# Kernel tuning notes

Hardware: AMD Instinct MI355X
Metric: run time of the kernel (lower is better)

## Reference

```python
import jax, jax.numpy as jnp
import numpy as np

B, S, E, H, MAXLEN = 2, 2048, 1024, 16, 2048


def _level_indices(seq_len: int, base: int = 2) -> np.ndarray:
    """Vectorized version of get_level_index_weak over the full (target, source) grid.
    indices[t, s] = min(level, 2) for s < t, else 0. Runs in O(log S) passes."""
    tt = np.broadcast_to(np.arange(seq_len)[:, None], (seq_len, seq_len)).astype(np.int64).copy()
    ss = np.broadcast_to(np.arange(seq_len)[None, :], (seq_len, seq_len)).astype(np.int64).copy()
    res = np.zeros((seq_len, seq_len), np.int64)
    done = ~(ss < tt)  # only source < target positions get a level; rest stay 0
    while not done.all():
        l = np.floor(np.log2(np.maximum(tt, 1).astype(np.float64))).astype(np.int64)
        v = (np.int64(1) << l)
        hit = (~done) & (ss < v)
        res[hit] = l[hit] + 1
        done |= hit
        step = ~done
        tt[step] -= v[step]
        ss[step] -= v[step]
    return np.minimum(res, 2).astype(np.int32)


def setup_inputs() -> dict:
    key = jax.random.key(0)
    ks = jax.random.split(key, 10)
    sc = 0.02
    return {
        "x": jax.random.normal(ks[0], (B, S, E), dtype=jnp.float32),
        "attention_mask": jax.random.randint(ks[1], (B, S), 0, 2, dtype=jnp.int32),
        "level_indices": jnp.asarray(_level_indices(S, 2)),
        "Wq": jax.random.normal(ks[2], (E, E), dtype=jnp.float32) * sc,
        "bq": jnp.zeros((E,), jnp.float32),
        "Wk": jax.random.normal(ks[3], (E, E), dtype=jnp.float32) * sc,
        "bk": jnp.zeros((E,), jnp.float32),
        "Wv": jax.random.normal(ks[4], (E, E), dtype=jnp.float32) * sc,
        "bv": jnp.zeros((E,), jnp.float32),
        "hier": jax.random.normal(ks[5], (MAXLEN, H, 3), dtype=jnp.float32),
        "Wo": jax.random.normal(ks[6], (E, E), dtype=jnp.float32) * sc,
        "bo": jnp.zeros((E,), jnp.float32),
    }


def reference(x, attention_mask, level_indices, Wq, bq, Wk, bk, Wv, bv, hier, Wo, bo):
    b, s, e = x.shape
    h = hier.shape[1]
    dh = e // h
    # q/k are computed by the original module but never used; kept for fidelity (zero grads).
    q = x @ Wq.T + bq
    k = x @ Wk.T + bk
    v = (x @ Wv.T + bv).reshape(b, s, h, dh).transpose(0, 2, 1, 3)  # [B,H,S,Dh]
    lev = level_indices[:s, :s]  # [S,S] int, values in {0,1,2}
    # Faithful torch.gather semantics: weights[b,h,i,j] = hier[b, h, lev[i,j]]
    w3 = hier[:b]                      # [B,H,3]
    weights = w3[:, :, lev]            # [B,H,S,S]
    decay = jnp.power(jnp.float32(0.5), lev.astype(x.dtype))  # [S,S]
    weights = weights * decay
    weights = weights / (jnp.sum(weights, axis=-1, keepdims=True) + 1e-8)
    weights = jnp.where(attention_mask[:, None, None, :] == 0, jnp.float32(0.0), weights)
    out = jnp.einsum('bhij,bhjd->bhid', weights, v)  # [B,H,S,Dh]
    out = out.transpose(0, 2, 1, 3).reshape(b, s, e)
    return out @ Wo.T + bo
```

## Files before the change

kernel.cpp:

```cpp
#include <hip/hip_runtime.h>
#include <cstdint>
#include <cstddef>

constexpr int Sn = 2048;
constexpr int En = 1024;
constexpr int Bn = 2;
constexpr int Hn = 16;
constexpr int CHUNK = 32;
constexpr int NCH = Sn / CHUNK;
constexpr int Mtot = Bn * Sn;
constexpr int GCH = Mtot / CHUNK;

typedef __bf16 bf16x8 __attribute__((ext_vector_type(8)));
typedef float  f32x4  __attribute__((ext_vector_type(4)));

__device__ __forceinline__ unsigned short f2bf(float f) {
    union { float f; uint32_t u; } v; v.f = f;
    const uint32_t u = v.u;
    return (unsigned short)((u + 0x7fffu + ((u >> 16) & 1u)) >> 16);
}
__device__ __forceinline__ float bf2f(unsigned short s) {
    union { uint32_t u; float f; } v; v.u = (uint32_t)s << 16; return v.f;
}

__device__ __forceinline__ void barrier_light() {
    asm volatile("s_waitcnt lgkmcnt(0)" ::: "memory");
    __builtin_amdgcn_s_barrier();
}

constexpr int XN = Bn * Sn * En;
constexpr int WN = En * En;

__global__ __launch_bounds__(256)
void cast2(const float* __restrict__ x, const float* __restrict__ Wv,
           unsigned short* __restrict__ xb, unsigned short* __restrict__ Wvb)
{
    const int i = (blockIdx.x * 256 + threadIdx.x) * 4;
    const float* src; unsigned short* dst; int off;
    if (i < XN) { src = x;  dst = xb;  off = i; }
    else        { src = Wv; dst = Wvb; off = i - XN; }
    const float4 v = *(const float4*)(src + off);
    ushort4 o;
    o.x = f2bf(v.x); o.y = f2bf(v.y); o.z = f2bf(v.z); o.w = f2bf(v.w);
    *(ushort4*)(dst + off) = o;
}

#define LOAD6(k0, r0, r1, r2, r3, r4, r5)            \
    r0 = *(const uint4*)(gA0 + (k0));                \
    r1 = *(const uint4*)(gA0 + (k0) + 32);           \
    r2 = *(const uint4*)(gA1 + (k0));                \
    r3 = *(const uint4*)(gA1 + (k0) + 32);           \
    r4 = *(const uint4*)(gB0 + (k0));                \
    r5 = *(const uint4*)(gB0 + (k0) + 32);

#define STORE6B(B, r0, r1, r2, r3, r4, r5)                       \
    *(uint4*)&As[B][(rg0 * 2 + 0) * 512 + lane * 8] = r0;        \
    *(uint4*)&As[B][(rg0 * 2 + 1) * 512 + lane * 8] = r1;        \
    *(uint4*)&As[B][(rg1 * 2 + 0) * 512 + lane * 8] = r2;        \
    *(uint4*)&As[B][(rg1 * 2 + 1) * 512 + lane * 8] = r3;        \
    *(uint4*)&Bs[B][(wv  * 2 + 0) * 512 + lane * 8] = r4;        \
    *(uint4*)&Bs[B][(wv  * 2 + 1) * 512 + lane * 8] = r5;

#define COMPUTEB(B)                                                                            \
    {                                                                                          \
        bf16x8 af[4][2], bfr[2][2];                                                            \
        _Pragma("unroll")                                                                      \
        for (int i = 0; i < 4; ++i)                                                            \
            _Pragma("unroll")                                                                  \
            for (int kh = 0; kh < 2; ++kh)                                                     \
                af[i][kh] = *(const bf16x8*)&As[B][((wr * 4 + i) * 2 + kh) * 512 + lane * 8];   \
        _Pragma("unroll")                                                                      \
        for (int j = 0; j < 2; ++j)                                                            \
            _Pragma("unroll")                                                                  \
            for (int kh = 0; kh < 2; ++kh)                                                     \
                bfr[j][kh] = *(const bf16x8*)&Bs[B][((wc * 2 + j) * 2 + kh) * 512 + lane * 8]; \
        _Pragma("unroll")                                                                      \
        for (int kh = 0; kh < 2; ++kh)                                                         \
            _Pragma("unroll")                                                                  \
            for (int i = 0; i < 4; ++i)                                                        \
                _Pragma("unroll")                                                              \
                for (int j = 0; j < 2; ++j)                                                    \
                    acc[i][j] = __builtin_amdgcn_mfma_f32_16x16x32_bf16(af[i][kh], bfr[j][kh], \
                                                                        acc[i][j], 0, 0, 0);   \
    }

template<bool APPLY_MASK, bool OUT_BF16, bool FUSE_CSUM>
__global__ __launch_bounds__(256)
void gemm_pipe(const unsigned short* __restrict__ A, const unsigned short* __restrict__ Bw,
               const float* __restrict__ bias, const int* __restrict__ mask,
               void* __restrict__ Cv, float* __restrict__ csum)
{
    __shared__ __align__(16) unsigned short As[2][128 * 64];
    __shared__ __align__(16) unsigned short Bs[2][64 * 64];

    const int tid  = threadIdx.x;
    const int lane = tid & 63;
    const int wv   = tid >> 6;
    const int wr   = wv >> 1;
    const int wc   = wv & 1;
    const int id   = blockIdx.y * 16 + blockIdx.x;
    const int xcd  = id & 7;
    const int slot = id >> 3;
    const int by   = xcd * 4 + (slot >> 4);
    const int bx   = slot & 15;
    const int bm   = by * 128;
    const int bn   = bx * 64;
    const int m16  = lane & 15;
    const int kq   = lane >> 4;

    f32x4 acc[4][2] = {};

    const int rg0 = 2 * wv, rg1 = 2 * wv + 1;
    const unsigned short* gA0 = A  + (size_t)(bm + 16 * rg0 + m16) * En + kq * 8;
    const unsigned short* gA1 = A  + (size_t)(bm + 16 * rg1 + m16) * En + kq * 8;
    const unsigned short* gB0 = Bw + (size_t)(bn + 16 * wv  + m16) * En + kq * 8;

    uint4 p0, p1, p2, p3, p4, p5;
    uint4 q0, q1, q2, q3, q4, q5;

    LOAD6(0,  p0, p1, p2, p3, p4, p5);
    STORE6B(0, p0, p1, p2, p3, p4, p5);
    LOAD6(64, q0, q1, q2, q3, q4, q5);
    barrier_light();

#pragma unroll 1
    for (int it = 0; it < 7; ++it) {
        const int kb = it * 128;
        LOAD6(kb + 128, p0, p1, p2, p3, p4, p5);
        COMPUTEB(0);
        STORE6B(1, q0, q1, q2, q3, q4, q5);
        barrier_light();
        LOAD6(kb + 192, q0, q1, q2, q3, q4, q5);
        COMPUTEB(1);
        STORE6B(0, p0, p1, p2, p3, p4, p5);
        barrier_light();
    }
    COMPUTEB(0);
    STORE6B(1, q0, q1, q2, q3, q4, q5);
    barrier_light();
    COMPUTEB(1);

    float colsum[2][2] = {{0.0f, 0.0f}, {0.0f, 0.0f}};
#pragma unroll
    for (int i = 0; i < 4; ++i) {
        const int r0_ = bm + wr * 64 + i * 16 + kq * 4;
#pragma unroll
        for (int j = 0; j < 2; ++j) {
            const int c0 = bn + wc * 32 + j * 16 + m16;
            const float bcol = bias[c0];
#pragma unroll
            for (int r = 0; r < 4; ++r) {
                const int row = r0_ + r;
                float val = acc[i][j][r] + bcol;
                if (APPLY_MASK) val = (mask[row] == 0) ? 0.0f : val;
                if (FUSE_CSUM) colsum[i >> 1][j] += val;
                if (OUT_BF16)
                    ((unsigned short*)Cv)[(size_t)row * En + c0] = f2bf(val);
                else
                    ((float*)Cv)[(size_t)row * En + c0] = val;
            }
        }
    }

    if (FUSE_CSUM) {
        const int gc0 = 4 * by + 2 * wr;
#pragma unroll
        for (int g = 0; g < 2; ++g)
#pragma unroll
            for (int j = 0; j < 2; ++j) {
                float s = colsum[g][j];
                s += __shfl_xor(s, 16, 64);
                s += __shfl_xor(s, 32, 64);
                if (kq == 0)
                    csum[(size_t)(gc0 + g) * En + bn + wc * 32 + j * 16 + m16] = s;
            }
    }
}

__global__ __launch_bounds__(256)
void combine(const unsigned short* __restrict__ vm, const float* __restrict__ csum,
             const float* __restrict__ hier, const float* __restrict__ Wo,
             unsigned short* __restrict__ Wob, unsigned short* __restrict__ opre)
{
    __shared__ __align__(16) unsigned short tile[CHUNK * 256];

    const int tid = threadIdx.x;
    const int ec0 = blockIdx.x * 256;
    const int c   = blockIdx.y;
    const int b   = blockIdx.z;

    {
        const int lane16 = tid & 31;
        const int rbase  = tid >> 5;
        const size_t g0 = ((size_t)b * Sn + c * CHUNK) * En + ec0 + lane16 * 8;
#pragma unroll
        for (int r4 = 0; r4 < 4; ++r4) {
            const int row = r4 * 8 + rbase;
            *(uint4*)&tile[row * 256 + lane16 * 8] =
                *(const uint4*)(vm + g0 + (size_t)row * En);
        }
    }

    {
        const int fid = (blockIdx.z * 64 + blockIdx.y) * 4 + blockIdx.x;
        const int base = fid * 2048 + tid * 4;
#pragma unroll
        for (int half = 0; half < 2; ++half) {
            const int off = base + half * 1024;
            const float4 v = *(const float4*)(Wo + off);
            ushort4 o;
            o.x = f2bf(v.x); o.y = f2bf(v.y); o.z = f2bf(v.z); o.w = f2bf(v.w);
            *(ushort4*)(Wob + off) = o;
        }
    }

    const int e = ec0 + tid;
    const int h = e >> 6;
    const float w0 = hier[((size_t)b * Hn + h) * 3 + 0];
    const float w1 = hier[((size_t)b * Hn + h) * 3 + 1] * 0.5f;
    const float w2 = hier[((size_t)b * Hn + h) * 3 + 2] * 0.25f;

    float run = 0.0f, T = 0.0f;
    {
        const float* cp = csum + (size_t)b * NCH * En + e;
#pragma unroll 16
        for (int c2 = 0; c2 < NCH; ++c2) {
            const float v = cp[(size_t)c2 * En];
            T += v;
            run += (c2 < c) ? v : 0.0f;
        }
    }

    __syncthreads();

    float prev = 0.0f;
    const size_t base = ((size_t)b * Sn + c * CHUNK) * En + e;

#pragma unroll
    for (int t = 0; t < CHUNK; ++t) {
        const int i = c * CHUNK + t;
        const float cur = bf2f(tile[t * 256 + tid]);
        float num, Z;
        if (i & 1) {
            num = w2 * (run - prev) + w1 * prev + w0 * (T - run);
            Z = (float)(i - 1) * w2 + w1 + (float)(Sn - i) * w0 + 1e-8f;
        } else {
            num = w2 * run + w0 * (T - run);
            Z = (float)i * w2 + (float)(Sn - i) * w0 + 1e-8f;
        }
        opre[base + (size_t)t * En] = f2bf(num / Z);
        run += cur;
        prev = cur;
    }
}

extern "C" void kernel_launch(void* const* d_in, const int* in_sizes, int n_in,
                              void* d_out, int out_size, void* d_ws, size_t ws_size,
                              hipStream_t stream)
{
    const float* x    = (const float*)d_in[0];
    const int*   mask = (const int*)d_in[1];
    const float* Wv   = (const float*)d_in[7];
    const float* bv   = (const float*)d_in[8];
    const float* hier = (const float*)d_in[9];
    const float* Wo   = (const float*)d_in[10];
    const float* bo   = (const float*)d_in[11];
    float* out = (float*)d_out;

    char* ws = (char*)d_ws;
    unsigned short* xb    = (unsigned short*)ws;  ws += (size_t)Mtot * En * 2;
    unsigned short* Wvb   = (unsigned short*)ws;  ws += (size_t)En * En * 2;
    unsigned short* Wob   = (unsigned short*)ws;  ws += (size_t)En * En * 2;
    unsigned short* vmb   = (unsigned short*)ws;  ws += (size_t)Mtot * En * 2;
    float*          csum  = (float*)ws;           ws += (size_t)GCH * En * 4;
    unsigned short* opreb = (unsigned short*)ws;  ws += (size_t)Mtot * En * 2;

    dim3 threads(256);

    cast2<<<dim3((XN + WN) / 1024), threads, 0, stream>>>(x, Wv, xb, Wvb);

    dim3 gemm_grid(16, 32);

    gemm_pipe<true, true, true><<<gemm_grid, threads, 0, stream>>>(xb, Wvb, bv, mask, vmb, csum);
    combine<<<dim3(En / 256, NCH, Bn), threads, 0, stream>>>(vmb, csum, hier, Wo, Wob, opreb);
    gemm_pipe<false, false, false><<<gemm_grid, threads, 0, stream>>>(opreb, Wob, bo, nullptr, out, nullptr);
}
```

Before: 164.1 us.

## Split-K the V projection GEMM into two halves summed in combine

The first GEMM (x·Wv) is split along K into two halves, run as a z-dimension of the grid, so the grid doubles from 512 to 1024 blocks and keeps more of the 256 CUs busy. Each half writes its own bf16 partial V and partial column sums, and the combine kernel adds the two partials while loading its tile, which now holds fp32 values. This trades extra workspace traffic (a second V buffer and csum buffer) and an extra bf16 rounding per partial for better occupancy of the first GEMM.

Result: slower. 170.3 us (+3.8%).

```diff
diff --git a/kernel.cpp b/kernel.cpp
--- a/kernel.cpp
+++ b/kernel.cpp
@@ -84,11 +84,11 @@
                                                                         acc[i][j], 0, 0, 0);   \
     }
 
-template<bool APPLY_MASK, bool OUT_BF16, bool FUSE_CSUM>
 __global__ __launch_bounds__(256)
-void gemm_pipe(const unsigned short* __restrict__ A, const unsigned short* __restrict__ Bw,
-               const float* __restrict__ bias, const int* __restrict__ mask,
-               void* __restrict__ Cv, float* __restrict__ csum)
+void gemm1_sk(const unsigned short* __restrict__ A, const unsigned short* __restrict__ Bw,
+              const float* __restrict__ bias, const int* __restrict__ mask,
+              unsigned short* __restrict__ vm0, unsigned short* __restrict__ vm1,
+              float* __restrict__ csum0, float* __restrict__ csum1)
 {
     __shared__ __align__(16) unsigned short As[2][128 * 64];
     __shared__ __align__(16) unsigned short Bs[2][64 * 64];
@@ -107,6 +107,99 @@
     const int bn   = bx * 64;
     const int m16  = lane & 15;
     const int kq   = lane >> 4;
+    const int ks   = blockIdx.z;
+
+    f32x4 acc[4][2] = {};
+
+    const int rg0 = 2 * wv, rg1 = 2 * wv + 1;
+    const size_t koff = (size_t)ks * 512;
+    const unsigned short* gA0 = A  + (size_t)(bm + 16 * rg0 + m16) * En + koff + kq * 8;
+    const unsigned short* gA1 = A  + (size_t)(bm + 16 * rg1 + m16) * En + koff + kq * 8;
+    const unsigned short* gB0 = Bw + (size_t)(bn + 16 * wv  + m16) * En + koff + kq * 8;
+
+    uint4 p0, p1, p2, p3, p4, p5;
+    uint4 q0, q1, q2, q3, q4, q5;
+
+    LOAD6(0,  p0, p1, p2, p3, p4, p5);
+    STORE6B(0, p0, p1, p2, p3, p4, p5);
+    LOAD6(64, q0, q1, q2, q3, q4, q5);
+    barrier_light();
+
+#pragma unroll 1
+    for (int it = 0; it < 3; ++it) {
+        const int kb = it * 128;
+        LOAD6(kb + 128, p0, p1, p2, p3, p4, p5);
+        COMPUTEB(0);
+        STORE6B(1, q0, q1, q2, q3, q4, q5);
+        barrier_light();
+        LOAD6(kb + 192, q0, q1, q2, q3, q4, q5);
+        COMPUTEB(1);
+        STORE6B(0, p0, p1, p2, p3, p4, p5);
+        barrier_light();
+    }
+    COMPUTEB(0);
+    STORE6B(1, q0, q1, q2, q3, q4, q5);
+    barrier_light();
+    COMPUTEB(1);
+
+    unsigned short* vmk = ks ? vm1 : vm0;
+    float*          csk = ks ? csum1 : csum0;
+    float colsum[2][2] = {{0.0f, 0.0f}, {0.0f, 0.0f}};
+#pragma unroll
+    for (int i = 0; i < 4; ++i) {
+        const int r0_ = bm + wr * 64 + i * 16 + kq * 4;
+#pragma unroll
+        for (int j = 0; j < 2; ++j) {
+            const int c0 = bn + wc * 32 + j * 16 + m16;
+            const float bcol = (ks == 0) ? bias[c0] : 0.0f;
+#pragma unroll
+            for (int r = 0; r < 4; ++r) {
+                const int row = r0_ + r;
+                float val = acc[i][j][r] + bcol;
+                val = (mask[row] == 0) ? 0.0f : val;
+                colsum[i >> 1][j] += val;
+                vmk[(size_t)row * En + c0] = f2bf(val);
+            }
+        }
+    }
+    {
+        const int gc0 = 4 * by + 2 * wr;
+#pragma unroll
+        for (int g = 0; g < 2; ++g)
+#pragma unroll
+            for (int j = 0; j < 2; ++j) {
+                float s = colsum[g][j];
+                s += __shfl_xor(s, 16, 64);
+                s += __shfl_xor(s, 32, 64);
+                if (kq == 0)
+                    csk[(size_t)(gc0 + g) * En + bn + wc * 32 + j * 16 + m16] = s;
+            }
+    }
+}
+
+template<bool APPLY_MASK, bool OUT_BF16, bool FUSE_CSUM>
+__global__ __launch_bounds__(256)
+void gemm_pipe(const unsigned short* __restrict__ A, const unsigned short* __restrict__ Bw,
+               const float* __restrict__ bias, const int* __restrict__ mask,
+               void* __restrict__ Cv, float* __restrict__ csum)
+{
+    __shared__ __align__(16) unsigned short As[2][128 * 64];
+    __shared__ __align__(16) unsigned short Bs[2][64 * 64];
+
+    const int tid  = threadIdx.x;
+    const int lane = tid & 63;
+    const int wv   = tid >> 6;
+    const int wr   = wv >> 1;
+    const int wc   = wv & 1;
+    const int id   = blockIdx.y * 16 + blockIdx.x;
+    const int xcd  = id & 7;
+    const int slot = id >> 3;
+    const int by   = xcd * 4 + (slot >> 4);
+    const int bx   = slot & 15;
+    const int bm   = by * 128;
+    const int bn   = bx * 64;
+    const int m16  = lane & 15;
+    const int kq   = lane >> 4;
 
     f32x4 acc[4][2] = {};
 
@@ -178,11 +271,12 @@
 }
 
 __global__ __launch_bounds__(256)
-void combine(const unsigned short* __restrict__ vm, const float* __restrict__ csum,
+void combine(const unsigned short* __restrict__ vm0, const unsigned short* __restrict__ vm1,
+             const float* __restrict__ csum0, const float* __restrict__ csum1,
              const float* __restrict__ hier, const float* __restrict__ Wo,
              unsigned short* __restrict__ Wob, unsigned short* __restrict__ opre)
 {
-    __shared__ __align__(16) unsigned short tile[CHUNK * 256];
+    __shared__ __align__(16) float tilef[CHUNK * 256];
 
     const int tid = threadIdx.x;
     const int ec0 = blockIdx.x * 256;
@@ -196,8 +290,14 @@
 #pragma unroll
         for (int r4 = 0; r4 < 4; ++r4) {
             const int row = r4 * 8 + rbase;
-            *(uint4*)&tile[row * 256 + lane16 * 8] =
-                *(const uint4*)(vm + g0 + (size_t)row * En);
+            const uint4 va = *(const uint4*)(vm0 + g0 + (size_t)row * En);
+            const uint4 vb = *(const uint4*)(vm1 + g0 + (size_t)row * En);
+            const unsigned short* pa = (const unsigned short*)&va;
+            const unsigned short* pb = (const unsigned short*)&vb;
+            float* d = &tilef[row * 256 + lane16 * 8];
+#pragma unroll
+            for (int k = 0; k < 8; ++k)
+                d[k] = bf2f(pa[k]) + bf2f(pb[k]);
         }
     }
 
@@ -222,10 +322,11 @@
 
     float run = 0.0f, T = 0.0f;
     {
-        const float* cp = csum + (size_t)b * NCH * En + e;
+        const float* cp0 = csum0 + (size_t)b * NCH * En + e;
+        const float* cp1 = csum1 + (size_t)b * NCH * En + e;
 #pragma unroll 16
         for (int c2 = 0; c2 < NCH; ++c2) {
-            const float v = cp[(size_t)c2 * En];
+            const float v = cp0[(size_t)c2 * En] + cp1[(size_t)c2 * En];
             T += v;
             run += (c2 < c) ? v : 0.0f;
         }
@@ -239,7 +340,7 @@
 #pragma unroll
     for (int t = 0; t < CHUNK; ++t) {
         const int i = c * CHUNK + t;
-        const float cur = bf2f(tile[t * 256 + tid]);
+        const float cur = tilef[t * 256 + tid];
         float num, Z;
         if (i & 1) {
             num = w2 * (run - prev) + w1 * prev + w0 * (T - run);
@@ -271,17 +372,20 @@
     unsigned short* xb    = (unsigned short*)ws;  ws += (size_t)Mtot * En * 2;
     unsigned short* Wvb   = (unsigned short*)ws;  ws += (size_t)En * En * 2;
     unsigned short* Wob   = (unsigned short*)ws;  ws += (size_t)En * En * 2;
-    unsigned short* vmb   = (unsigned short*)ws;  ws += (size_t)Mtot * En * 2;
-    float*          csum  = (float*)ws;           ws += (size_t)GCH * En * 4;
+    unsigned short* vmb0  = (unsigned short*)ws;  ws += (size_t)Mtot * En * 2;
+    unsigned short* vmb1  = (unsigned short*)ws;  ws += (size_t)Mtot * En * 2;
+    float*          csum0 = (float*)ws;           ws += (size_t)GCH * En * 4;
+    float*          csum1 = (float*)ws;           ws += (size_t)GCH * En * 4;
     unsigned short* opreb = (unsigned short*)ws;  ws += (size_t)Mtot * En * 2;
 
     dim3 threads(256);
 
     cast2<<<dim3((XN + WN) / 1024), threads, 0, stream>>>(x, Wv, xb, Wvb);
 
-    dim3 gemm_grid(16, 32);
-
-    gemm_pipe<true, true, true><<<gemm_grid, threads, 0, stream>>>(xb, Wvb, bv, mask, vmb, csum);
-    combine<<<dim3(En / 256, NCH, Bn), threads, 0, stream>>>(vmb, csum, hier, Wo, Wob, opreb);
-    gemm_pipe<false, false, false><<<gemm_grid, threads, 0, stream>>>(opreb, Wob, bo, nullptr, out, nullptr);
-}
+    gemm1_sk<<<dim3(16, 32, 2), threads, 0, stream>>>(xb, Wvb, bv, mask,
+                                                      vmb0, vmb1, csum0, csum1);
+    combine<<<dim3(En / 256, NCH, Bn), threads, 0, stream>>>(vmb0, vmb1, csum0, csum1,
+                                                             hier, Wo, Wob, opreb);
+    gemm_pipe<false, false, false><<<dim3(16, 32), threads, 0, stream>>>(opreb, Wob, bo,
+                                                                         nullptr, out, nullptr);
+}
```
